# Kernel optimization log

Measured on AMD Instinct MI355X. Metric: run time of the kernel, lower is better.

Reference implementation:

```python
import jax, jax.numpy as jnp
import numpy as np

B, D, K = 32768, 512, 5
SIM_THRESH = 0.7
GATE_TEMP = 1.0
LN_EPS = 1e-5


def setup_inputs() -> dict:
    key = jax.random.key(0)
    ks = jax.random.split(key, 12)
    s = 1.0 / np.sqrt(D)
    query = jax.random.normal(ks[0], (B, D), dtype=jnp.float32)
    retrieved_memories = jax.random.normal(ks[1], (B, K, D), dtype=jnp.float32)
    similarities = jax.random.uniform(ks[2], (B, K), dtype=jnp.float32)
    mask = jax.random.randint(ks[3], (B, K), 0, 2) > 0
    mask = mask.at[:, 0].set(True)  # at least one valid memory per row
    return {
        "query": query,
        "retrieved_memories": retrieved_memories,
        "similarities": similarities,
        "mask": mask,
        "Wq": jax.random.normal(ks[4], (D, D), dtype=jnp.float32) * s,
        "bq": jnp.zeros((D,), jnp.float32),
        "Wk": jax.random.normal(ks[5], (D, D), dtype=jnp.float32) * s,
        "bk": jnp.zeros((D,), jnp.float32),
        "Wv": jax.random.normal(ks[6], (D, D), dtype=jnp.float32) * s,
        "bv": jnp.zeros((D,), jnp.float32),
        "Wo": jax.random.normal(ks[7], (D, D), dtype=jnp.float32) * s,
        "bo": jnp.zeros((D,), jnp.float32),
        "Wg": jax.random.normal(ks[8], (2 * D, 1), dtype=jnp.float32) * s,
        "bg": jnp.zeros((1,), jnp.float32),
        "ln_g": jnp.ones((D,), jnp.float32),
        "ln_b": jnp.zeros((D,), jnp.float32),
    }


def reference(query, retrieved_memories, similarities, mask,
              Wq, bq, Wk, bk, Wv, bv, Wo, bo, Wg, bg, ln_g, ln_b):
    scale = D ** (-0.5)
    q = query @ Wq + bq                                          # (B, D)
    k = jnp.einsum('bkd,de->bke', retrieved_memories, Wk) + bk   # (B, K, D)
    v = jnp.einsum('bkd,de->bke', retrieved_memories, Wv) + bv   # (B, K, D)
    scores = jnp.einsum('bd,bkd->bk', q, k) * scale              # (B, K)
    scores = jnp.where(mask, scores, -jnp.inf)
    w = jax.nn.softmax(scores, axis=-1)
    w = jnp.where(mask, w, 0.0)
    mem = jnp.einsum('bk,bkd->bd', w, v)                         # (B, D)
    mem = mem @ Wo + bo
    # gated fusion
    max_sim = jnp.max(similarities, axis=-1, keepdims=True)      # (B, 1)
    gate = jax.nn.sigmoid(jnp.concatenate([query, mem], axis=-1) @ Wg + bg)
    conf = jax.nn.sigmoid(GATE_TEMP * (max_sim - SIM_THRESH))
    out = query + (gate * conf) * mem
    # layer norm
    mu = jnp.mean(out, axis=-1, keepdims=True)
    var = jnp.mean((out - mu) ** 2, axis=-1, keepdims=True)
    out = (out - mu) * jax.lax.rsqrt(var + LN_EPS) * ln_g + ln_b
    return out
```

## Files before the change

### kernel.cpp

```cpp
#include <hip/hip_runtime.h>

#define DD 512
#define KM 5
#define B_ROWS 32768

typedef __attribute__((ext_vector_type(8))) short short8;
typedef __attribute__((ext_vector_type(4))) short s16x4;
typedef __attribute__((ext_vector_type(4))) float f32x4;

static __device__ __forceinline__ short f2bf(float x) {
  unsigned u = __builtin_bit_cast(unsigned, x);
  u = (u + 0x7fffu + ((u >> 16) & 1u)) >> 16;
  return (short)u;
}
static __device__ __forceinline__ float bf2f(short s) {
  unsigned u = ((unsigned)(unsigned short)s) << 16;
  return __builtin_bit_cast(float, u);
}

#define BAR_LGKM() do { asm volatile("s_waitcnt lgkmcnt(0)" ::: "memory"); __builtin_amdgcn_s_barrier(); } while (0)

__global__ __launch_bounds__(512, 2)
void prepG(const float* __restrict__ Wq, const float* __restrict__ bq,
           const float* __restrict__ Wk, const float* __restrict__ Wv,
           const float* __restrict__ Wo, const float* __restrict__ bo,
           const float* __restrict__ bv,
           short* __restrict__ At, short* __restrict__ Ct,
           float* __restrict__ w0, float* __restrict__ d0) {
  __shared__ short sh[12288];
  const int tid = threadIdx.x;
  const int blk = blockIdx.x;
  if (blk < 64) {
    const bool isC = blk >= 32;
    const int b = blk & 31;
    const int j0 = (b >> 3) * 128;
    const int i0 = (b & 7) * 64;
    const int lane = tid & 63;
    const int w = tid >> 6;
    const int wm = w & 1, wn = w >> 1;
    const int kg = lane >> 4, lr = lane & 15;
    const float* Ysrc = isC ? Wv : Wq;
    f32x4 acc[4] = {};
    f32x4 ra0, ra1;
    f32x4 rbv;
    if (!isC) {
      const float* p = Wk + (size_t)(j0 + (tid >> 2)) * DD + (tid & 3) * 8;
      ra0 = *(const f32x4*)p; ra1 = *(const f32x4*)(p + 4);
    } else {
      const float* p = Wo + (size_t)(tid >> 4) * DD + j0 + (tid & 15) * 8;
      ra0 = *(const f32x4*)p; ra1 = *(const f32x4*)(p + 4);
    }
    rbv = *(const f32x4*)(Ysrc + (size_t)(i0 + (tid >> 3)) * DD + (tid & 7) * 4);
    for (int ki = 0; ki < 16; ++ki) {
      short* As = (ki & 1) ? (sh + 4096) : sh;
      short* Bs = (ki & 1) ? (sh + 10240) : (sh + 8192);
      if (!isC) {
        short8 sv;
        sv[0]=f2bf(ra0[0]); sv[1]=f2bf(ra0[1]); sv[2]=f2bf(ra0[2]); sv[3]=f2bf(ra0[3]);
        sv[4]=f2bf(ra1[0]); sv[5]=f2bf(ra1[1]); sv[6]=f2bf(ra1[2]); sv[7]=f2bf(ra1[3]);
        *(short8*)&As[(tid >> 2) * 32 + (((tid & 3) * 8) ^ (((tid >> 2) & 3) << 3))] = sv;
      } else {
        const int e = tid >> 4;
#pragma unroll
        for (int c = 0; c < 8; ++c) {
          const int j = (tid & 15) * 8 + c;
          const float v = (c < 4) ? ra0[c & 3] : ra1[c & 3];
          As[j * 32 + (e ^ ((j & 3) << 3))] = f2bf(v);
        }
      }
      {
        s16x4 sv;
        sv[0]=f2bf(rbv[0]); sv[1]=f2bf(rbv[1]); sv[2]=f2bf(rbv[2]); sv[3]=f2bf(rbv[3]);
        *(s16x4*)&Bs[(tid >> 3) * 32 + (((tid & 7) * 4) ^ (((tid >> 3) & 3) << 3))] = sv;
      }
      if (ki < 15) {
        const int kt = (ki + 1) * 32;
        if (!isC) {
          const float* p = Wk + (size_t)(j0 + (tid >> 2)) * DD + kt + (tid & 3) * 8;
          ra0 = *(const f32x4*)p; ra1 = *(const f32x4*)(p + 4);
        } else {
          const float* p = Wo + (size_t)(kt + (tid >> 4)) * DD + j0 + (tid & 15) * 8;
          ra0 = *(const f32x4*)p; ra1 = *(const f32x4*)(p + 4);
        }
        rbv = *(const f32x4*)(Ysrc + (size_t)(i0 + (tid >> 3)) * DD + kt + (tid & 7) * 4);
      }
      __syncthreads();
      short8 av[4], bvv;
#pragma unroll
      for (int mi = 0; mi < 4; ++mi) {
        const int ar = wm * 64 + mi * 16 + lr;
        av[mi] = *(const short8*)&As[ar * 32 + ((kg * 8) ^ ((lr & 3) << 3))];
      }
      {
        const int br = wn * 16 + lr;
        bvv = *(const short8*)&Bs[br * 32 + ((kg * 8) ^ ((lr & 3) << 3))];
      }
#pragma unroll
      for (int mi = 0; mi < 4; ++mi)
        acc[mi] = __builtin_amdgcn_mfma_f32_16x16x32_bf16(av[mi], bvv, acc[mi], 0, 0, 0);
      __syncthreads();
    }
    short* P = isC ? Ct : At;
    const int cwl = wn * 16 + lr;
    const int kiv = (b & 7) * 2 + (cwl >> 5);
    const int kkv = cwl & 31;
#pragma unroll
    for (int mi = 0; mi < 4; ++mi)
#pragma unroll
      for (int r = 0; r < 4; ++r) {
        const int j = j0 + wm * 64 + mi * 16 + kg * 4 + r;
        P[(size_t)kiv * 16384 + j * 32 + kkv] = f2bf(acc[mi][r]);
      }
  } else if (blk < 128) {
    const int j = (blk - 64) * 8 + (tid >> 6);
    const int lane = tid & 63;
    const float* r = Wk + (size_t)j * DD + lane * 8;
    f32x4 a = *(const f32x4*)r;
    f32x4 c = *(const f32x4*)(r + 4);
    const float* bp = bq + lane * 8;
    f32x4 ba = *(const f32x4*)bp;
    f32x4 bc = *(const f32x4*)(bp + 4);
    float s = a[0]*ba[0] + a[1]*ba[1] + a[2]*ba[2] + a[3]*ba[3]
            + c[0]*bc[0] + c[1]*bc[1] + c[2]*bc[2] + c[3]*bc[3];
#pragma unroll
    for (int off = 32; off > 0; off >>= 1) s += __shfl_xor(s, off);
    if (lane == 0) w0[j] = s;
  } else {
    float* red = (float*)sh;
    const int j = (blk - 128) * 256 + (tid & 255);
    const int half = tid >> 8;
    float s = 0.f;
    for (int e = half * 256; e < half * 256 + 256; ++e)
      s += bv[e] * Wo[(size_t)e * DD + j];
    red[half * 256 + (tid & 255)] = s;
    __syncthreads();
    if (half == 0) d0[j] = red[tid] + red[256 + tid] + bo[j];
  }
}

#define WRITE_A(DST, QLO, QHI) do {                                                \
  short8 _sv;                                                                      \
  _sv[0]=f2bf((QLO)[0]); _sv[1]=f2bf((QLO)[1]); _sv[2]=f2bf((QLO)[2]); _sv[3]=f2bf((QLO)[3]); \
  _sv[4]=f2bf((QHI)[0]); _sv[5]=f2bf((QHI)[1]); _sv[6]=f2bf((QHI)[2]); _sv[7]=f2bf((QHI)[3]); \
  *(short8*)&(DST)[arow * 32 + (acol ^ ((arow & 3) << 3))] = _sv; } while (0)

#define G1ITER(KI, ASC, ASN, BC, BN) do {                                   \
    short8 av[8];                                                           \
    _Pragma("unroll") for (int mi = 0; mi < 8; ++mi) {                      \
      const int ar = mi * 16 + lr;                                          \
      av[mi] = *(const short8*)&(ASC)[ar * 32 + ((kg * 8) ^ ((lr & 3) << 3))]; \
    }                                                                       \
    if ((KI) < 15) { WRITE_A(ASN, qA, qB); }                                \
    if ((KI) < 15) {                                                        \
      _Pragma("unroll") for (int ni = 0; ni < 4; ++ni)                      \
        (BN)[ni] = *(const short8*)(atb + ((KI) + 1) * 16384 + ni * 512);   \
    }                                                                       \
    if ((KI) < 14) {                                                        \
      qA = *(const f32x4*)(qbase + ((KI) + 2) * 32);                        \
      qB = *(const f32x4*)(qbase + ((KI) + 2) * 32 + 4);                    \
    }                                                                       \
    _Pragma("unroll") for (int mi = 0; mi < 8; ++mi)                        \
      _Pragma("unroll") for (int ni = 0; ni < 4; ++ni)                      \
        acc[mi][ni] = __builtin_amdgcn_mfma_f32_16x16x32_bf16(av[mi], (BC)[ni], acc[mi][ni], 0, 0, 0); \
    BAR_LGKM();                                                             \
  } while (0)

#define G2ITER(KI, BC, BN) do {                                             \
    short8 av[8];                                                           \
    _Pragma("unroll") for (int mi = 0; mi < 8; ++mi) {                      \
      const int ar = mi * 16 + lr;                                          \
      av[mi] = *(const short8*)&R1[(ar * DD + (KI) * 32 + kg * 8) ^ ((ar & 7) << 3)]; \
    }                                                                       \
    if ((KI) < 15) {                                                        \
      _Pragma("unroll") for (int ni = 0; ni < 4; ++ni)                      \
        (BN)[ni] = *(const short8*)(ctb + ((KI) + 1) * 16384 + ni * 512);   \
    }                                                                       \
    _Pragma("unroll") for (int mi = 0; mi < 8; ++mi)                        \
      _Pragma("unroll") for (int ni = 0; ni < 4; ++ni)                      \
        acc2[mi][ni] = __builtin_amdgcn_mfma_f32_16x16x32_bf16(av[mi], (BC)[ni], acc2[mi][ni], 0, 0, 0); \
  } while (0)

#define ROW_FINISH(SV, MA, MC, VM, ROW)                                     \
    {                                                                       \
      float mx = -1e30f;                                                    \
      _Pragma("unroll") for (int k = 0; k < KM; ++k)                        \
        if ((VM) & (1 << k)) mx = fmaxf(mx, SV[k]);                         \
      float wk[KM]; float sum = 0.f;                                        \
      _Pragma("unroll") for (int k = 0; k < KM; ++k) {                      \
        wk[k] = ((VM) & (1 << k)) ? __expf(SV[k] - mx) : 0.f;               \
        sum += wk[k];                                                       \
      }                                                                     \
      const float inv = 1.f / sum;                                          \
      float o[8] = {0.f,0.f,0.f,0.f,0.f,0.f,0.f,0.f};                       \
      _Pragma("unroll") for (int k = 0; k < KM; ++k)                        \
        if ((VM) & (1 << k)) {                                              \
          const float g = wk[k] * inv;                                      \
          _Pragma("unroll") for (int i = 0; i < 4; ++i) {                   \
            o[i] += g * MA[k][i]; o[4 + i] += g * MC[k][i];                 \
          }                                                                 \
        }                                                                   \
      short8 ov;                                                            \
      _Pragma("unroll") for (int i = 0; i < 8; ++i) ov[i] = f2bf(o[i]);     \
      *(short8*)&R1[((ROW) * DD + lane * 8) ^ (((ROW) & 7) << 3)] = ov;     \
    }

__global__ __launch_bounds__(512, 2)
void mk(const float* __restrict__ q, const short* __restrict__ AtP,
        const float* __restrict__ w0, const float* __restrict__ mem,
        const int* __restrict__ mask, const short* __restrict__ CtP,
        const float* __restrict__ d0, const float* __restrict__ sims,
        const float* __restrict__ Wg, const float* __restrict__ bgp,
        const float* __restrict__ lng, const float* __restrict__ lnb,
        float* __restrict__ outp) {
  __shared__ short R1[128 * DD];
  const int tid = threadIdx.x;
  const int lane = tid & 63;
  const int w = tid >> 6;
  const int kg = lane >> 4, lr = lane & 15;
  const int bm = blockIdx.x;

  short* As0 = R1;
  short* As1 = R1 + 4096;

  const short* atb = AtP + (size_t)(w * 64 + lr) * 32 + kg * 8;
  const short* ctb = CtP + (size_t)(w * 64 + lr) * 32 + kg * 8;

  f32x4 acc[8][4] = {};
  const int arow = tid >> 2, acol = (tid & 3) * 8;
  const float* qbase = q + (size_t)(bm * 128 + arow) * DD + acol;
  {
    f32x4 qA = *(const f32x4*)qbase;
    f32x4 qB = *(const f32x4*)(qbase + 4);
    WRITE_A(As0, qA, qB);
    qA = *(const f32x4*)(qbase + 32);
    qB = *(const f32x4*)(qbase + 36);
    short8 bA[4], bB[4];
#pragma unroll
    for (int ni = 0; ni < 4; ++ni) bA[ni] = *(const short8*)(atb + ni * 512);
    BAR_LGKM();
    for (int kp = 0; kp < 8; ++kp) {
      G1ITER(2 * kp,     As0, As1, bA, bB);
      G1ITER(2 * kp + 1, As1, As0, bB, bA);
    }
  }
#pragma unroll
  for (int ni = 0; ni < 4; ++ni) {
    const int col = w * 64 + ni * 16 + lr;
    const float b0 = w0[col];
#pragma unroll
    for (int mi = 0; mi < 8; ++mi)
#pragma unroll
      for (int r = 0; r < 4; ++r)
        R1[(mi * 16 + kg * 4 + r) * DD + col] = f2bf(acc[mi][ni][r] + b0);
  }
  BAR_LGKM();
  const float scale = 0.044194173824159216f;
  for (int rr = 0; rr < 16; rr += 2) {
    const int row0 = w * 16 + rr;
    const size_t b0 = (size_t)bm * 128 + row0;
    const short8 tv0 = *(const short8*)&R1[row0 * DD + lane * 8];
    const short8 tv1 = *(const short8*)&R1[(row0 + 1) * DD + lane * 8];
    float tf0[8], tf1[8];
#pragma unroll
    for (int i = 0; i < 8; ++i) { tf0[i] = bf2f(tv0[i]); tf1[i] = bf2f(tv1[i]); }
    int vm0 = 0, vm1 = 0;
#pragma unroll
    for (int k = 0; k < KM; ++k) {
      vm0 |= (__builtin_amdgcn_readfirstlane(mask[b0 * KM + k]) ? 1 : 0) << k;
      vm1 |= (__builtin_amdgcn_readfirstlane(mask[(b0 + 1) * KM + k]) ? 1 : 0) << k;
    }
    f32x4 ma0[KM], mc0[KM], ma1[KM], mc1[KM];
#pragma unroll
    for (int k = 0; k < KM; ++k) {
      if (vm0 & (1 << k)) {
        const f32x4* mp = (const f32x4*)(mem + (b0 * KM + k) * DD + lane * 8);
        ma0[k] = __builtin_nontemporal_load(mp);
        mc0[k] = __builtin_nontemporal_load(mp + 1);
      }
      if (vm1 & (1 << k)) {
        const f32x4* mp = (const f32x4*)(mem + ((b0 + 1) * KM + k) * DD + lane * 8);
        ma1[k] = __builtin_nontemporal_load(mp);
        mc1[k] = __builtin_nontemporal_load(mp + 1);
      }
    }
    float s0[KM], s1[KM];
#pragma unroll
    for (int k = 0; k < KM; ++k) {
      if (vm0 & (1 << k)) {
        float p = 0.f;
#pragma unroll
        for (int i = 0; i < 4; ++i) { p += tf0[i] * ma0[k][i]; p += tf0[4 + i] * mc0[k][i]; }
#pragma unroll
        for (int off = 32; off > 0; off >>= 1) p += __shfl_xor(p, off);
        s0[k] = p * scale;
      }
      if (vm1 & (1 << k)) {
        float p = 0.f;
#pragma unroll
        for (int i = 0; i < 4; ++i) { p += tf1[i] * ma1[k][i]; p += tf1[4 + i] * mc1[k][i]; }
#pragma unroll
        for (int off = 32; off > 0; off >>= 1) p += __shfl_xor(p, off);
        s1[k] = p * scale;
      }
    }
    ROW_FINISH(s0, ma0, mc0, vm0, row0)
    ROW_FINISH(s1, ma1, mc1, vm1, (row0 + 1))
  }
  BAR_LGKM();
  f32x4 acc2[8][4] = {};
  {
    short8 cA[4], cB[4];
#pragma unroll
    for (int ni = 0; ni < 4; ++ni) cA[ni] = *(const short8*)(ctb + ni * 512);
    for (int kp = 0; kp < 8; ++kp) {
      G2ITER(2 * kp,     cA, cB);
      G2ITER(2 * kp + 1, cB, cA);
    }
  }
  BAR_LGKM();
#pragma unroll
  for (int ni = 0; ni < 4; ++ni) {
    const int col = w * 64 + ni * 16 + lr;
    const float b0 = d0[col];
#pragma unroll
    for (int mi = 0; mi < 8; ++mi)
#pragma unroll
      for (int r = 0; r < 4; ++r)
        R1[(mi * 16 + kg * 4 + r) * DD + col] = f2bf(acc2[mi][ni][r] + b0);
  }
  BAR_LGKM();
  {
    const float* wg1 = Wg + lane * 8;
    const float* wg2 = Wg + DD + lane * 8;
    f32x4 g1a = *(const f32x4*)wg1, g1b = *(const f32x4*)(wg1 + 4);
    f32x4 g2a = *(const f32x4*)wg2, g2b = *(const f32x4*)(wg2 + 4);
    f32x4 la = *(const f32x4*)(lng + lane * 8), lb4 = *(const f32x4*)(lng + lane * 8 + 4);
    f32x4 ba = *(const f32x4*)(lnb + lane * 8), bb4 = *(const f32x4*)(lnb + lane * 8 + 4);
    const float bgs = bgp[0];
    for (int rr = 0; rr < 16; ++rr) {
      const int row = w * 16 + rr;
      const size_t b = (size_t)bm * 128 + row;
      const float* qp = q + b * DD + lane * 8;
      f32x4 q0 = *(const f32x4*)qp;
      f32x4 q1 = *(const f32x4*)(qp + 4);
      float qf[8] = {q0[0],q0[1],q0[2],q0[3],q1[0],q1[1],q1[2],q1[3]};
      const short8 mv = *(const short8*)&R1[row * DD + lane * 8];
      float mf[8];
#pragma unroll
      for (int i = 0; i < 8; ++i) mf[i] = bf2f(mv[i]);
      float gp = qf[0]*g1a[0]+qf[1]*g1a[1]+qf[2]*g1a[2]+qf[3]*g1a[3]
               + qf[4]*g1b[0]+qf[5]*g1b[1]+qf[6]*g1b[2]+qf[7]*g1b[3]
               + mf[0]*g2a[0]+mf[1]*g2a[1]+mf[2]*g2a[2]+mf[3]*g2a[3]
               + mf[4]*g2b[0]+mf[5]*g2b[1]+mf[6]*g2b[2]+mf[7]*g2b[3];
#pragma unroll
      for (int off = 32; off > 0; off >>= 1) gp += __shfl_xor(gp, off);
      const float gate = 1.f / (1.f + __expf(-(gp + bgs)));
      float ms = sims[b * KM];
#pragma unroll
      for (int k = 1; k < KM; ++k) ms = fmaxf(ms, sims[b * KM + k]);
      const float conf = 1.f / (1.f + __expf(-(ms - 0.7f)));
      const float gc = gate * conf;
      float o[8];
      float s1 = 0.f, s2 = 0.f;
#pragma unroll
      for (int i = 0; i < 8; ++i) {
        o[i] = qf[i] + gc * mf[i];
        s1 += o[i];
        s2 += o[i] * o[i];
      }
#pragma unroll
      for (int off = 32; off > 0; off >>= 1) { s1 += __shfl_xor(s1, off); s2 += __shfl_xor(s2, off); }
      const float mu = s1 * (1.f / 512.f);
      const float var = s2 * (1.f / 512.f) - mu * mu;
      const float rs = rsqrtf(var + 1e-5f);
      f32x4 r0, r1;
#pragma unroll
      for (int i = 0; i < 4; ++i) r0[i] = (o[i] - mu) * rs * la[i] + ba[i];
#pragma unroll
      for (int i = 0; i < 4; ++i) r1[i] = (o[4 + i] - mu) * rs * lb4[i] + bb4[i];
      float* op = outp + b * DD + lane * 8;
      __builtin_nontemporal_store(r0, (f32x4*)op);
      __builtin_nontemporal_store(r1, (f32x4*)(op + 4));
    }
  }
}

extern "C" void kernel_launch(void* const* d_in, const int* in_sizes, int n_in,
                              void* d_out, int out_size, void* d_ws, size_t ws_size,
                              hipStream_t stream) {
  const float* query = (const float*)d_in[0];
  const float* mem   = (const float*)d_in[1];
  const float* sims  = (const float*)d_in[2];
  const int*   mask  = (const int*)d_in[3];
  const float* Wq = (const float*)d_in[4];
  const float* bq = (const float*)d_in[5];
  const float* Wk = (const float*)d_in[6];
  const float* Wv = (const float*)d_in[8];
  const float* bv = (const float*)d_in[9];
  const float* Wo = (const float*)d_in[10];
  const float* bo = (const float*)d_in[11];
  const float* Wg = (const float*)d_in[12];
  const float* bg = (const float*)d_in[13];
  const float* ln_g = (const float*)d_in[14];
  const float* ln_b = (const float*)d_in[15];
  float* out = (float*)d_out;

  char* ws = (char*)d_ws;
  short* AtP = (short*)ws;
  short* CtP = AtP + (size_t)DD * DD;
  float* w0 = (float*)(CtP + (size_t)DD * DD);
  float* d0 = w0 + DD;

  prepG<<<dim3(130), dim3(512), 0, stream>>>(Wq, bq, Wk, Wv, Wo, bo, bv, AtP, CtP, w0, d0);
  mk<<<dim3(B_ROWS / 128), dim3(512), 0, stream>>>(query, AtP, w0, mem, mask,
                                                   CtP, d0, sims, Wg, bg, ln_g, ln_b, out);
}
```

Measured before the change: 130.5 us.

## Halve row tile to 64 per block and double occupancy to four blocks

```diff
diff --git a/kernel.cpp b/kernel.cpp
--- a/kernel.cpp
+++ b/kernel.cpp
@@ -138,46 +138,39 @@
   }
 }
 
-#define WRITE_A(DST, QLO, QHI) do {                                                \
-  short8 _sv;                                                                      \
-  _sv[0]=f2bf((QLO)[0]); _sv[1]=f2bf((QLO)[1]); _sv[2]=f2bf((QLO)[2]); _sv[3]=f2bf((QLO)[3]); \
-  _sv[4]=f2bf((QHI)[0]); _sv[5]=f2bf((QHI)[1]); _sv[6]=f2bf((QHI)[2]); _sv[7]=f2bf((QHI)[3]); \
-  *(short8*)&(DST)[arow * 32 + (acol ^ ((arow & 3) << 3))] = _sv; } while (0)
-
-#define G1ITER(KI, ASC, ASN, BC, BN) do {                                   \
-    short8 av[8];                                                           \
-    _Pragma("unroll") for (int mi = 0; mi < 8; ++mi) {                      \
+#define WRITE_A4(DST, QV) do {                                              \
+  s16x4 _sv;                                                                \
+  _sv[0]=f2bf((QV)[0]); _sv[1]=f2bf((QV)[1]);                               \
+  _sv[2]=f2bf((QV)[2]); _sv[3]=f2bf((QV)[3]);                               \
+  *(s16x4*)&(DST)[arow * 32 + (acol ^ ((arow & 3) << 3))] = _sv; } while (0)
+
+#define G1ITER(KI, ASC, ASN) do {                                           \
+    short8 av[4], bv[4];                                                    \
+    _Pragma("unroll") for (int ni = 0; ni < 4; ++ni)                        \
+      bv[ni] = *(const short8*)(atb + (KI) * 16384 + ni * 512);             \
+    _Pragma("unroll") for (int mi = 0; mi < 4; ++mi) {                      \
       const int ar = mi * 16 + lr;                                          \
       av[mi] = *(const short8*)&(ASC)[ar * 32 + ((kg * 8) ^ ((lr & 3) << 3))]; \
     }                                                                       \
-    if ((KI) < 15) { WRITE_A(ASN, qA, qB); }                                \
-    if ((KI) < 15) {                                                        \
+    if ((KI) < 15) { WRITE_A4(ASN, qA); }                                   \
+    if ((KI) < 14) { qA = *(const f32x4*)(qbase + ((KI) + 2) * 32); }       \
+    _Pragma("unroll") for (int mi = 0; mi < 4; ++mi)                        \
       _Pragma("unroll") for (int ni = 0; ni < 4; ++ni)                      \
-        (BN)[ni] = *(const short8*)(atb + ((KI) + 1) * 16384 + ni * 512);   \
-    }                                                                       \
-    if ((KI) < 14) {                                                        \
-      qA = *(const f32x4*)(qbase + ((KI) + 2) * 32);                        \
-      qB = *(const f32x4*)(qbase + ((KI) + 2) * 32 + 4);                    \
-    }                                                                       \
-    _Pragma("unroll") for (int mi = 0; mi < 8; ++mi)                        \
-      _Pragma("unroll") for (int ni = 0; ni < 4; ++ni)                      \
-        acc[mi][ni] = __builtin_amdgcn_mfma_f32_16x16x32_bf16(av[mi], (BC)[ni], acc[mi][ni], 0, 0, 0); \
+        acc[mi][ni] = __builtin_amdgcn_mfma_f32_16x16x32_bf16(av[mi], bv[ni], acc[mi][ni], 0, 0, 0); \
     BAR_LGKM();                                                             \
   } while (0)
 
-#define G2ITER(KI, BC, BN) do {                                             \
-    short8 av[8];                                                           \
-    _Pragma("unroll") for (int mi = 0; mi < 8; ++mi) {                      \
+#define G2ITER(KI) do {                                                     \
+    short8 av[4], cv[4];                                                    \
+    _Pragma("unroll") for (int ni = 0; ni < 4; ++ni)                        \
+      cv[ni] = *(const short8*)(ctb + (KI) * 16384 + ni * 512);             \
+    _Pragma("unroll") for (int mi = 0; mi < 4; ++mi) {                      \
       const int ar = mi * 16 + lr;                                          \
       av[mi] = *(const short8*)&R1[(ar * DD + (KI) * 32 + kg * 8) ^ ((ar & 7) << 3)]; \
     }                                                                       \
-    if ((KI) < 15) {                                                        \
+    _Pragma("unroll") for (int mi = 0; mi < 4; ++mi)                        \
       _Pragma("unroll") for (int ni = 0; ni < 4; ++ni)                      \
-        (BN)[ni] = *(const short8*)(ctb + ((KI) + 1) * 16384 + ni * 512);   \
-    }                                                                       \
-    _Pragma("unroll") for (int mi = 0; mi < 8; ++mi)                        \
-      _Pragma("unroll") for (int ni = 0; ni < 4; ++ni)                      \
-        acc2[mi][ni] = __builtin_amdgcn_mfma_f32_16x16x32_bf16(av[mi], (BC)[ni], acc2[mi][ni], 0, 0, 0); \
+        acc2[mi][ni] = __builtin_amdgcn_mfma_f32_16x16x32_bf16(av[mi], cv[ni], acc2[mi][ni], 0, 0, 0); \
   } while (0)
 
 #define ROW_FINISH(SV, MA, MC, VM, ROW)                                     \
@@ -204,7 +197,7 @@
       *(short8*)&R1[((ROW) * DD + lane * 8) ^ (((ROW) & 7) << 3)] = ov;     \
     }
 
-__global__ __launch_bounds__(512, 2)
+__global__ __launch_bounds__(512, 4)
 void mk(const float* __restrict__ q, const short* __restrict__ AtP,
         const float* __restrict__ w0, const float* __restrict__ mem,
         const int* __restrict__ mask, const short* __restrict__ CtP,
@@ -212,7 +205,7 @@
         const float* __restrict__ Wg, const float* __restrict__ bgp,
         const float* __restrict__ lng, const float* __restrict__ lnb,
         float* __restrict__ outp) {
-  __shared__ short R1[128 * DD];
+  __shared__ short R1[64 * DD];
   const int tid = threadIdx.x;
   const int lane = tid & 63;
   const int w = tid >> 6;
@@ -220,27 +213,22 @@
   const int bm = blockIdx.x;
 
   short* As0 = R1;
-  short* As1 = R1 + 4096;
+  short* As1 = R1 + 2048;
 
   const short* atb = AtP + (size_t)(w * 64 + lr) * 32 + kg * 8;
   const short* ctb = CtP + (size_t)(w * 64 + lr) * 32 + kg * 8;
 
-  f32x4 acc[8][4] = {};
-  const int arow = tid >> 2, acol = (tid & 3) * 8;
-  const float* qbase = q + (size_t)(bm * 128 + arow) * DD + acol;
+  f32x4 acc[4][4] = {};
+  const int arow = tid >> 3, acol = (tid & 7) * 4;
+  const float* qbase = q + (size_t)(bm * 64 + arow) * DD + acol;
   {
     f32x4 qA = *(const f32x4*)qbase;
-    f32x4 qB = *(const f32x4*)(qbase + 4);
-    WRITE_A(As0, qA, qB);
+    WRITE_A4(As0, qA);
     qA = *(const f32x4*)(qbase + 32);
-    qB = *(const f32x4*)(qbase + 36);
-    short8 bA[4], bB[4];
-#pragma unroll
-    for (int ni = 0; ni < 4; ++ni) bA[ni] = *(const short8*)(atb + ni * 512);
     BAR_LGKM();
     for (int kp = 0; kp < 8; ++kp) {
-      G1ITER(2 * kp,     As0, As1, bA, bB);
-      G1ITER(2 * kp + 1, As1, As0, bB, bA);
+      G1ITER(2 * kp,     As0, As1);
+      G1ITER(2 * kp + 1, As1, As0);
     }
   }
 #pragma unroll
@@ -248,82 +236,55 @@
     const int col = w * 64 + ni * 16 + lr;
     const float b0 = w0[col];
 #pragma unroll
-    for (int mi = 0; mi < 8; ++mi)
+    for (int mi = 0; mi < 4; ++mi)
 #pragma unroll
       for (int r = 0; r < 4; ++r)
         R1[(mi * 16 + kg * 4 + r) * DD + col] = f2bf(acc[mi][ni][r] + b0);
   }
   BAR_LGKM();
   const float scale = 0.044194173824159216f;
-  for (int rr = 0; rr < 16; rr += 2) {
-    const int row0 = w * 16 + rr;
-    const size_t b0 = (size_t)bm * 128 + row0;
-    const short8 tv0 = *(const short8*)&R1[row0 * DD + lane * 8];
-    const short8 tv1 = *(const short8*)&R1[(row0 + 1) * DD + lane * 8];
-    float tf0[8], tf1[8];
-#pragma unroll
-    for (int i = 0; i < 8; ++i) { tf0[i] = bf2f(tv0[i]); tf1[i] = bf2f(tv1[i]); }
-    int vm0 = 0, vm1 = 0;
-#pragma unroll
-    for (int k = 0; k < KM; ++k) {
-      vm0 |= (__builtin_amdgcn_readfirstlane(mask[b0 * KM + k]) ? 1 : 0) << k;
-      vm1 |= (__builtin_amdgcn_readfirstlane(mask[(b0 + 1) * KM + k]) ? 1 : 0) << k;
-    }
-    f32x4 ma0[KM], mc0[KM], ma1[KM], mc1[KM];
-#pragma unroll
-    for (int k = 0; k < KM; ++k) {
-      if (vm0 & (1 << k)) {
-        const f32x4* mp = (const f32x4*)(mem + (b0 * KM + k) * DD + lane * 8);
-        ma0[k] = __builtin_nontemporal_load(mp);
-        mc0[k] = __builtin_nontemporal_load(mp + 1);
-      }
-      if (vm1 & (1 << k)) {
-        const f32x4* mp = (const f32x4*)(mem + ((b0 + 1) * KM + k) * DD + lane * 8);
-        ma1[k] = __builtin_nontemporal_load(mp);
-        mc1[k] = __builtin_nontemporal_load(mp + 1);
-      }
-    }
-    float s0[KM], s1[KM];
-#pragma unroll
-    for (int k = 0; k < KM; ++k) {
-      if (vm0 & (1 << k)) {
+  for (int rr = 0; rr < 8; ++rr) {
+    const int row = w * 8 + rr;
+    const size_t b = (size_t)bm * 64 + row;
+    const short8 tv = *(const short8*)&R1[row * DD + lane * 8];
+    float tf[8];
+#pragma unroll
+    for (int i = 0; i < 8; ++i) tf[i] = bf2f(tv[i]);
+    int vm = 0;
+#pragma unroll
+    for (int k = 0; k < KM; ++k)
+      vm |= (__builtin_amdgcn_readfirstlane(mask[b * KM + k]) ? 1 : 0) << k;
+    f32x4 ma[KM], mc[KM];
+#pragma unroll
+    for (int k = 0; k < KM; ++k)
+      if (vm & (1 << k)) {
+        const f32x4* mp = (const f32x4*)(mem + (b * KM + k) * DD + lane * 8);
+        ma[k] = __builtin_nontemporal_load(mp);
+        mc[k] = __builtin_nontemporal_load(mp + 1);
+      }
+    float s[KM];
+#pragma unroll
+    for (int k = 0; k < KM; ++k)
+      if (vm & (1 << k)) {
         float p = 0.f;
 #pragma unroll
-        for (int i = 0; i < 4; ++i) { p += tf0[i] * ma0[k][i]; p += tf0[4 + i] * mc0[k][i]; }
+        for (int i = 0; i < 4; ++i) { p += tf[i] * ma[k][i]; p += tf[4 + i] * mc[k][i]; }
 #pragma unroll
         for (int off = 32; off > 0; off >>= 1) p += __shfl_xor(p, off);
-        s0[k] = p * scale;
-      }
-      if (vm1 & (1 << k)) {
-        float p = 0.f;
-#pragma unroll
-        for (int i = 0; i < 4; ++i) { p += tf1[i] * ma1[k][i]; p += tf1[4 + i] * mc1[k][i]; }
-#pragma unroll
-        for (int off = 32; off > 0; off >>= 1) p += __shfl_xor(p, off);
-        s1[k] = p * scale;
-      }
-    }
-    ROW_FINISH(s0, ma0, mc0, vm0, row0)
-    ROW_FINISH(s1, ma1, mc1, vm1, (row0 + 1))
+        s[k] = p * scale;
+      }
+    ROW_FINISH(s, ma, mc, vm, row)
   }
   BAR_LGKM();
-  f32x4 acc2[8][4] = {};
-  {
-    short8 cA[4], cB[4];
-#pragma unroll
-    for (int ni = 0; ni < 4; ++ni) cA[ni] = *(const short8*)(ctb + ni * 512);
-    for (int kp = 0; kp < 8; ++kp) {
-      G2ITER(2 * kp,     cA, cB);
-      G2ITER(2 * kp + 1, cB, cA);
-    }
-  }
+  f32x4 acc2[4][4] = {};
+  for (int ki = 0; ki < 16; ++ki) G2ITER(ki);
   BAR_LGKM();
 #pragma unroll
   for (int ni = 0; ni < 4; ++ni) {
     const int col = w * 64 + ni * 16 + lr;
     const float b0 = d0[col];
 #pragma unroll
-    for (int mi = 0; mi < 8; ++mi)
+    for (int mi = 0; mi < 4; ++mi)
 #pragma unroll
       for (int r = 0; r < 4; ++r)
         R1[(mi * 16 + kg * 4 + r) * DD + col] = f2bf(acc2[mi][ni][r] + b0);
@@ -337,9 +298,9 @@
     f32x4 la = *(const f32x4*)(lng + lane * 8), lb4 = *(const f32x4*)(lng + lane * 8 + 4);
     f32x4 ba = *(const f32x4*)(lnb + lane * 8), bb4 = *(const f32x4*)(lnb + lane * 8 + 4);
     const float bgs = bgp[0];
-    for (int rr = 0; rr < 16; ++rr) {
-      const int row = w * 16 + rr;
-      const size_t b = (size_t)bm * 128 + row;
+    for (int rr = 0; rr < 8; ++rr) {
+      const int row = w * 8 + rr;
+      const size_t b = (size_t)bm * 64 + row;
       const float* qp = q + b * DD + lane * 8;
       f32x4 q0 = *(const f32x4*)qp;
       f32x4 q1 = *(const f32x4*)(qp + 4);
@@ -412,6 +373,6 @@
   float* d0 = w0 + DD;
 
   prepG<<<dim3(130), dim3(512), 0, stream>>>(Wq, bq, Wk, Wv, Wo, bo, bv, AtP, CtP, w0, d0);
-  mk<<<dim3(B_ROWS / 128), dim3(512), 0, stream>>>(query, AtP, w0, mem, mask,
-                                                   CtP, d0, sims, Wg, bg, ln_g, ln_b, out);
-}
+  mk<<<dim3(B_ROWS / 64), dim3(512), 0, stream>>>(query, AtP, w0, mem, mask,
+                                                  CtP, d0, sims, Wg, bg, ln_g, ln_b, out);
+}
```

Measured after the change: 135.7 us. +3.9%, slower.
